# Optimization experiments

Hardware: AMD Instinct MI355X
Metric: run time of the kernel (lower is better)

Reference implementation:

```python
import jax, jax.numpy as jnp
import numpy as np

B, N, D = 4, 2048, 512
H, DA, DL = 8, 64, 64  # heads, attention_dim, linear_dim
EPS = 1e-6


def _layer_norm(x, eps=EPS):
    # F.layer_norm with no affine params
    mu = jnp.mean(x, axis=-1, keepdims=True)
    var = jnp.var(x, axis=-1, keepdims=True)
    return (x - mu) * jax.lax.rsqrt(var + eps)


def setup_inputs() -> dict:
    key = jax.random.key(0)
    k1, k2, k3, k4 = jax.random.split(key, 4)
    x = jax.random.normal(k1, (B, N, D), dtype=jnp.float32)
    # causal (lower-triangular) valid-attention mask, float {0,1}, shape (B,1,N,N)
    attention_mask = jnp.broadcast_to(
        jnp.tril(jnp.ones((N, N), dtype=jnp.float32))[None, None], (B, 1, N, N)
    )
    # _uvqk: (D, 2*H*DL + 2*H*DA), init normal(0, 0.02)
    uvqk = 0.02 * jax.random.normal(k2, (D, 2 * H * DL + 2 * H * DA), dtype=jnp.float32)
    # _o: Linear(H*DL -> D), xavier uniform
    fan_in, fan_out = H * DL, D
    limit = float(np.sqrt(6.0 / (fan_in + fan_out)))
    o_weight = jax.random.uniform(k3, (fan_out, fan_in), dtype=jnp.float32, minval=-limit, maxval=limit)
    o_bias = jnp.zeros((D,), dtype=jnp.float32)
    return {"x": x, "attention_mask": attention_mask, "uvqk": uvqk,
            "o_weight": o_weight, "o_bias": o_bias}


def reference(x, attention_mask, uvqk, o_weight, o_bias):
    b, n, _ = x.shape
    normed_x = _layer_norm(x)
    mm = jax.nn.silu(normed_x @ uvqk)  # fused uvqk projection + silu
    u, v, q, k = jnp.split(mm, [H * DL, 2 * H * DL, 2 * H * DL + H * DA], axis=-1)
    qh = q.reshape(b, n, H, DA)
    kh = k.reshape(b, n, H, DA)
    vh = v.reshape(b, n, H, DL)
    # silu-activated (non-softmax) attention with mask
    qk = jnp.einsum('bnhd,bmhd->bhnm', qh, kh)
    qk = jax.nn.silu(qk) / n
    qk = qk * attention_mask  # (B,1,N,N) broadcast over heads
    attn = jnp.einsum('bhnm,bmhd->bnhd', qk, vh).reshape(b, n, H * DL)
    # gated norm + output proj + residual
    o_input = u * _layer_norm(attn)
    return o_input @ o_weight.T + o_bias + x
```

## Files before the change

### kernel.cpp

```cpp
#include <hip/hip_runtime.h>

typedef __bf16 bf16x8 __attribute__((ext_vector_type(8)));
typedef float f32x4 __attribute__((ext_vector_type(4)));
typedef float f32x16 __attribute__((ext_vector_type(16)));
typedef int i32x2 __attribute__((ext_vector_type(2)));

__device__ __forceinline__ unsigned short f2bf(float f) {
  return __builtin_bit_cast(unsigned short, (__bf16)f);
}
__device__ __forceinline__ float bfu2f(unsigned short b) {
  unsigned int u = ((unsigned int)b) << 16;
  return __builtin_bit_cast(float, u);
}
__device__ __forceinline__ float silu_f(float x) {
  return x * __builtin_amdgcn_rcpf(1.0f + __expf(-x));
}
__device__ __forceinline__ unsigned pk2(float a, float b) {
  return (unsigned)f2bf(a) | ((unsigned)f2bf(b) << 16);
}

template<int CPR, int NI, int SWZ>
__device__ __forceinline__ void stage16(const __bf16* __restrict__ g, int ld,
                                        __bf16* lds, int wave, int lane) {
#pragma unroll
  for (int t = 0; t < NI; ++t) {
    int cb = (wave * NI + t) * 64;
    int c = cb + lane;
    int row = c / CPR;
    int colb = (c % CPR) ^ (row & SWZ);
    __builtin_amdgcn_global_load_lds(
        (const __attribute__((address_space(1))) unsigned int*)(g + row * ld + colb * 8),
        (__attribute__((address_space(3))) unsigned int*)(lds + cb * 8),
        16, 0, 0);
  }
}

__global__ void k_prep(const float* __restrict__ x, __bf16* __restrict__ nx,
                       const float* __restrict__ ow, __bf16* __restrict__ owb,
                       const float* __restrict__ uvqk, __bf16* __restrict__ uvqkT) {
  int bid = blockIdx.x, tid = threadIdx.x;
  if (bid < 4096) {
    int t = tid & 127;
    int r = bid * 2 + (tid >> 7);
    int wave = tid >> 6;
    float4 v = ((const float4*)(x + (size_t)r * 512))[t];
    float s = v.x + v.y + v.z + v.w;
    float ss = v.x * v.x + v.y * v.y + v.z * v.z + v.w * v.w;
#pragma unroll
    for (int o = 32; o > 0; o >>= 1) { s += __shfl_down(s, o); ss += __shfl_down(ss, o); }
    __shared__ float red[4][2];
    if ((tid & 63) == 0) { red[wave][0] = s; red[wave][1] = ss; }
    __syncthreads();
    int rw = (wave >> 1) * 2;
    s = red[rw][0] + red[rw + 1][0];
    ss = red[rw][1] + red[rw + 1][1];
    float mu = s * (1.0f / 512.0f);
    float var = ss * (1.0f / 512.0f) - mu * mu;
    float rs = rsqrtf(var + 1e-6f);
    ushort4 o4;
    o4.x = f2bf((v.x - mu) * rs); o4.y = f2bf((v.y - mu) * rs);
    o4.z = f2bf((v.z - mu) * rs); o4.w = f2bf((v.w - mu) * rs);
    ((ushort4*)(nx + (size_t)r * 512))[t] = o4;
  } else if (bid < 4352) {
    int i = (bid - 4096) * 256 + tid;
    float4 v = ((const float4*)ow)[i];
    ushort4 o4;
    o4.x = f2bf(v.x); o4.y = f2bf(v.y); o4.z = f2bf(v.z); o4.w = f2bf(v.w);
    ((ushort4*)owb)[i] = o4;
  } else {
    __shared__ float tile[32][33];
    int bb = bid - 4352;
    int n0 = (bb & 63) * 32, k0 = (bb >> 6) * 32;
    int tx = tid & 31, ty = tid >> 5;
    for (int i = ty; i < 32; i += 8)
      tile[i][tx] = uvqk[(k0 + i) * 2048 + n0 + tx];
    __syncthreads();
    for (int i = ty; i < 32; i += 8)
      uvqkT[(n0 + i) * 512 + k0 + tx] = (__bf16)tile[tx][i];
  }
}

__global__ __launch_bounds__(256, 2) void k_proj(
    const __bf16* __restrict__ A, const __bf16* __restrict__ Bt,
    __bf16* __restrict__ u, __bf16* __restrict__ qn,
    __bf16* __restrict__ kn, __bf16* __restrict__ vt) {
  __shared__ __bf16 As[128 * 64];
  __shared__ __bf16 Bs[256 * 64];
  int tid = threadIdx.x, wave = tid >> 6, lane = tid & 63;
  int lr = lane & 15, lq = lane >> 4;
  int bn = blockIdx.x, bm = blockIdx.y;
  const __bf16* Ag = A + (size_t)bm * 128 * 512;
  const __bf16* Bg = Bt + (size_t)bn * 256 * 512;
  int wm = (wave >> 1) * 64, wn2 = (wave & 1) * 128;
  f32x4 acc[4][8] = {};
  for (int k0 = 0; k0 < 512; k0 += 64) {
    stage16<8, 4, 7>(Ag + k0, 512, As, wave, lane);
    stage16<8, 8, 7>(Bg + k0, 512, Bs, wave, lane);
    __syncthreads();
#pragma unroll
    for (int kk = 0; kk < 2; ++kk) {
      int b = kk * 4 + lq;
      bf16x8 a[4], bb[8];
#pragma unroll
      for (int i = 0; i < 4; ++i) {
        int row = wm + i * 16 + lr;
        a[i] = *(const bf16x8*)(As + row * 64 + ((b ^ (row & 7)) * 8));
      }
#pragma unroll
      for (int j = 0; j < 8; ++j) {
        int row = wn2 + j * 16 + lr;
        bb[j] = *(const bf16x8*)(Bs + row * 64 + ((b ^ (row & 7)) * 8));
      }
#pragma unroll
      for (int i = 0; i < 4; ++i)
#pragma unroll
        for (int j = 0; j < 8; ++j)
          acc[i][j] = __builtin_amdgcn_mfma_f32_16x16x32_bf16(a[i], bb[j], acc[i][j], 0, 0, 0);
    }
    __syncthreads();
  }
  int seg = bn >> 1;
  int cb = (bn & 1) * 256 + wn2;
  int rb0 = bm * 128 + wm + lq * 4;
  if (seg == 1) {
#pragma unroll
    for (int i = 0; i < 4; ++i) {
      int rb = rb0 + i * 16;
      int b = rb >> 11, n = rb & 2047;
#pragma unroll
      for (int j = 0; j < 8; ++j) {
        int c = cb + j * 16 + lr;
        ushort4 w;
        w.x = f2bf(silu_f(acc[i][j][0]) * (1.0f / 2048.0f));
        w.y = f2bf(silu_f(acc[i][j][1]) * (1.0f / 2048.0f));
        w.z = f2bf(silu_f(acc[i][j][2]) * (1.0f / 2048.0f));
        w.w = f2bf(silu_f(acc[i][j][3]) * (1.0f / 2048.0f));
        *(ushort4*)(vt + ((size_t)(b * 512 + c)) * 2048 + n) = w;
      }
    }
  } else {
    __bf16* dst = (seg == 0) ? u : ((seg == 2) ? qn : kn);
#pragma unroll
    for (int i = 0; i < 4; ++i) {
      int rb = rb0 + i * 16;
#pragma unroll
      for (int j = 0; j < 8; ++j) {
        int c = cb + j * 16 + lr;
#pragma unroll
        for (int rg = 0; rg < 4; ++rg)
          dst[(size_t)(rb + rg) * 512 + c] = (__bf16)silu_f(acc[i][j][rg]);
      }
    }
  }
}

template<bool DT>
__device__ __forceinline__ void attn_finish(
    const f32x16& s, int m0, int n0, int l31, int lh, int ms, bool natural,
    const __bf16* Vc, f32x16 po[2]) {
  unsigned pk[8];
#pragma unroll
  for (int q = 0; q < 8; ++q) {
    float p01[2];
#pragma unroll
    for (int h = 0; h < 2; ++h) {
      int r = 2 * q + h;
      float xx = s[r];
      float pv = xx * __builtin_amdgcn_rcpf(1.0f + __expf(-xx));
      if (DT) {
        int mrow = m0 + 4 * lh + (r & 3) + 8 * (r >> 2);
        if (mrow > n0 + l31) pv = 0.0f;
      }
      p01[h] = pv;
    }
    pk[q] = pk2(p01[0], p01[1]);
  }
  i32x2 r0 = __builtin_amdgcn_permlane32_swap((int)pk[0], (int)pk[2], false, false);
  i32x2 r1 = __builtin_amdgcn_permlane32_swap((int)pk[1], (int)pk[3], false, false);
  i32x2 r2 = __builtin_amdgcn_permlane32_swap((int)pk[4], (int)pk[6], false, false);
  i32x2 r3 = __builtin_amdgcn_permlane32_swap((int)pk[5], (int)pk[7], false, false);
  union { bf16x8 v; unsigned u[4]; } f0, f1;
  if (natural) {
    f0.u[0] = r0.x; f0.u[2] = r0.y; f0.u[1] = r1.x; f0.u[3] = r1.y;
    f1.u[0] = r2.x; f1.u[2] = r2.y; f1.u[1] = r3.x; f1.u[3] = r3.y;
  } else {
    f0.u[0] = r0.y; f0.u[2] = r0.x; f0.u[1] = r1.y; f0.u[3] = r1.x;
    f1.u[0] = r2.y; f1.u[2] = r2.x; f1.u[1] = r3.y; f1.u[3] = r3.x;
  }
  bf16x8 pf[2] = { f0.v, f1.v };
#pragma unroll
  for (int t2 = 0; t2 < 2; ++t2) {
#pragma unroll
    for (int idl = 0; idl < 2; ++idl) {
      int row = idl * 32 + l31;
      bf16x8 av = *(const bf16x8*)(Vc + row * 64 +
          (((ms * 4 + t2 * 2 + lh) ^ (row & 7)) * 8));
      po[idl] = __builtin_amdgcn_mfma_f32_32x32x16_bf16(av, pf[t2], po[idl], 0, 0, 0);
    }
  }
}

__global__ __launch_bounds__(256, 4) void k_attn(
    const __bf16* __restrict__ qn, const __bf16* __restrict__ kn,
    const __bf16* __restrict__ vt, __bf16* __restrict__ oa,
    __bf16* __restrict__ ob, __bf16* __restrict__ oc) {
  __shared__ __bf16 lds[16384];
  __bf16* Kb0 = lds;
  __bf16* Kb1 = lds + 4096;
  __bf16* Vb0 = lds + 8192;
  __bf16* Vb1 = lds + 12288;
  __bf16* bo = lds;

  int bh = blockIdx.x, p = blockIdx.y, z = blockIdx.z;
  int b = bh >> 3, hd = bh & 7;
  int tid = threadIdx.x, wave = tid >> 6, lane = tid & 63;
  int l31 = lane & 31, lh = lane >> 5;
  const __bf16* Kg = kn + (size_t)(b * 2048) * 512 + hd * 64;
  const __bf16* Vg = vt + (size_t)(b * 512 + hd * 64) * 2048;
  __bf16* Oz = (z == 0) ? oa : ((z == 1) ? ob : oc);

  i32x2 pr = __builtin_amdgcn_permlane32_swap(lh ? 10 : 11, lh ? 20 : 21, false, false);
  bool natural = (__builtin_amdgcn_readfirstlane(pr.x) == 11);

  for (int ph = 0; ph < 2; ++ph) {
    int t = ph ? (15 - p) : p;
    int T = 2 * t + 2;
    int mlo = z * T / 3;
    int cnt = (z + 1) * T / 3 - mlo;
    int n0 = t * 128 + wave * 32;
    if (ph) __syncthreads();
    const __bf16* Qg = qn + (size_t)(b * 2048 + n0 + l31) * 512 + hd * 64 + lh * 8;
    bf16x8 qf[4];
#pragma unroll
    for (int ks = 0; ks < 4; ++ks) qf[ks] = *(const bf16x8*)(Qg + ks * 16);
    if (cnt > 0) {
      stage16<8, 2, 7>(Kg + (size_t)mlo * 64 * 512, 512, Kb0, wave, lane);
      stage16<8, 2, 7>(Vg + mlo * 64, 2048, Vb0, wave, lane);
    }
    __syncthreads();

    f32x16 po[2] = {};

    for (int i = 0; i < cnt; ++i) {
      int mt = mlo + i;
      const __bf16* Kc = (i & 1) ? Kb1 : Kb0;
      const __bf16* Vc = (i & 1) ? Vb1 : Vb0;
      if (i + 1 < cnt) {
        __bf16* Kn_ = (i & 1) ? Kb0 : Kb1;
        __bf16* Vn_ = (i & 1) ? Vb0 : Vb1;
        stage16<8, 2, 7>(Kg + (size_t)(mt + 1) * 64 * 512, 512, Kn_, wave, lane);
        stage16<8, 2, 7>(Vg + (mt + 1) * 64, 2048, Vn_, wave, lane);
      }
#pragma unroll
      for (int ms = 0; ms < 2; ++ms) {
        int m0 = mt * 64 + ms * 32;
        if (m0 > n0) continue;
        f32x16 s = {};
#pragma unroll
        for (int ks = 0; ks < 4; ++ks) {
          int row = ms * 32 + l31;
          bf16x8 ak = *(const bf16x8*)(Kc + row * 64 + (((ks * 2 + lh) ^ (row & 7)) * 8));
          s = __builtin_amdgcn_mfma_f32_32x32x16_bf16(ak, qf[ks], s, 0, 0, 0);
        }
        if (m0 == n0) attn_finish<true>(s, m0, n0, l31, lh, ms, natural, Vc, po);
        else          attn_finish<false>(s, m0, n0, l31, lh, ms, natural, Vc, po);
      }
      __syncthreads();
    }

    {
      int nrow = wave * 32 + l31;
#pragma unroll
      for (int idl = 0; idl < 2; ++idl) {
#pragma unroll
        for (int g = 0; g < 4; ++g) {
          int dl0 = idl * 32 + g * 8 + lh * 4;
          int addr = nrow * 64 + ((((dl0 >> 3) ^ (nrow & 7)) << 3) | (dl0 & 7));
          ushort4 w;
          w.x = f2bf(po[idl][4 * g + 0]); w.y = f2bf(po[idl][4 * g + 1]);
          w.z = f2bf(po[idl][4 * g + 2]); w.w = f2bf(po[idl][4 * g + 3]);
          *(ushort4*)(bo + addr) = w;
        }
      }
    }
    __syncthreads();
    {
      int n = tid >> 1, cc = (tid & 1) * 32;
      __bf16* gdst = Oz + (size_t)(b * 2048 + t * 128 + n) * 512 + hd * 64 + cc;
#pragma unroll
      for (int kk2 = 0; kk2 < 4; ++kk2) {
        int dlb = cc + kk2 * 8;
        int a = n * 64 + (((dlb >> 3) ^ (n & 7)) << 3);
        *(uint4*)(gdst + kk2 * 8) = *(const uint4*)(bo + a);
      }
    }
  }
}

__global__ void k_oinput(const __bf16* __restrict__ oa, const __bf16* __restrict__ ob,
                         const __bf16* __restrict__ oc, const __bf16* __restrict__ u,
                         __bf16* __restrict__ oin) {
  int r = blockIdx.x, t = threadIdx.x;
  ushort4 a4 = ((const ushort4*)(oa + (size_t)r * 512))[t];
  ushort4 b4 = ((const ushort4*)(ob + (size_t)r * 512))[t];
  ushort4 c4 = ((const ushort4*)(oc + (size_t)r * 512))[t];
  float a0 = bfu2f(a4.x) + bfu2f(b4.x) + bfu2f(c4.x);
  float a1 = bfu2f(a4.y) + bfu2f(b4.y) + bfu2f(c4.y);
  float a2 = bfu2f(a4.z) + bfu2f(b4.z) + bfu2f(c4.z);
  float a3 = bfu2f(a4.w) + bfu2f(b4.w) + bfu2f(c4.w);
  float s = a0 + a1 + a2 + a3;
  float ss = a0 * a0 + a1 * a1 + a2 * a2 + a3 * a3;
#pragma unroll
  for (int o = 32; o > 0; o >>= 1) { s += __shfl_down(s, o); ss += __shfl_down(ss, o); }
  __shared__ float red[4];
  if ((t & 63) == 0) { red[(t >> 6) * 2] = s; red[(t >> 6) * 2 + 1] = ss; }
  __syncthreads();
  s = red[0] + red[2]; ss = red[1] + red[3];
  float mu = s * (1.0f / 512.0f);
  float var = ss * (1.0f / 512.0f) - mu * mu;
  float rs = rsqrtf(var + 1e-6f);
  ushort4 u4 = ((const ushort4*)(u + (size_t)r * 512))[t];
  ushort4 o4;
  o4.x = f2bf(bfu2f(u4.x) * (a0 - mu) * rs);
  o4.y = f2bf(bfu2f(u4.y) * (a1 - mu) * rs);
  o4.z = f2bf(bfu2f(u4.z) * (a2 - mu) * rs);
  o4.w = f2bf(bfu2f(u4.w) * (a3 - mu) * rs);
  ((ushort4*)(oin + (size_t)r * 512))[t] = o4;
}

__global__ __launch_bounds__(256, 4) void k_out(
    const __bf16* __restrict__ A, const __bf16* __restrict__ Bt,
    const float* __restrict__ bias, const float* __restrict__ x,
    float* __restrict__ out) {
  __shared__ __bf16 As[64 * 64];
  __shared__ __bf16 Bs[128 * 64];
  int tid = threadIdx.x, wave = tid >> 6, lane = tid & 63;
  int lr = lane & 15, lq = lane >> 4;
  int bn = blockIdx.x, bm = blockIdx.y;
  const __bf16* Ag = A + (size_t)bm * 64 * 512;
  const __bf16* Bg = Bt + (size_t)bn * 128 * 512;
  int wm = (wave >> 1) * 32, wn = (wave & 1) * 64;
  f32x4 acc[2][4] = {};
  for (int k0 = 0; k0 < 512; k0 += 64) {
    stage16<8, 2, 7>(Ag + k0, 512, As, wave, lane);
    stage16<8, 4, 7>(Bg + k0, 512, Bs, wave, lane);
    __syncthreads();
#pragma unroll
    for (int kk = 0; kk < 2; ++kk) {
      int b = kk * 4 + lq;
      bf16x8 a[2], bb[4];
#pragma unroll
      for (int i = 0; i < 2; ++i) {
        int row = wm + i * 16 + lr;
        a[i] = *(const bf16x8*)(As + row * 64 + ((b ^ (row & 7)) * 8));
      }
#pragma unroll
      for (int j = 0; j < 4; ++j) {
        int row = wn + j * 16 + lr;
        bb[j] = *(const bf16x8*)(Bs + row * 64 + ((b ^ (row & 7)) * 8));
      }
#pragma unroll
      for (int i = 0; i < 2; ++i)
#pragma unroll
        for (int j = 0; j < 4; ++j)
          acc[i][j] = __builtin_amdgcn_mfma_f32_16x16x32_bf16(a[i], bb[j], acc[i][j], 0, 0, 0);
    }
    __syncthreads();
  }
  int cb = bn * 128 + wn;
  int rb0 = bm * 64 + wm + lq * 4;
#pragma unroll
  for (int j = 0; j < 4; ++j) {
    int c = cb + j * 16 + lr;
    float bv = bias[c];
#pragma unroll
    for (int i = 0; i < 2; ++i) {
      int rb = rb0 + i * 16;
#pragma unroll
      for (int rg = 0; rg < 4; ++rg) {
        size_t idx = (size_t)(rb + rg) * 512 + c;
        out[idx] = acc[i][j][rg] + bv + x[idx];
      }
    }
  }
}

extern "C" void kernel_launch(void* const* d_in, const int* in_sizes, int n_in,
                              void* d_out, int out_size, void* d_ws, size_t ws_size,
                              hipStream_t stream) {
  const float* x = (const float*)d_in[0];
  const float* uvqk = (const float*)d_in[2];
  const float* ow = (const float*)d_in[3];
  const float* obias = (const float*)d_in[4];
  float* out = (float*)d_out;

  char* w = (char*)d_ws;
  const size_t MB8 = 8u * 1024 * 1024;
  __bf16* nx    = (__bf16*)(w);
  __bf16* u     = (__bf16*)(w + MB8);
  __bf16* qn    = (__bf16*)(w + 2 * MB8);
  __bf16* kn    = (__bf16*)(w + 3 * MB8);
  __bf16* vt    = (__bf16*)(w + 4 * MB8);
  __bf16* uvqkT = (__bf16*)(w + 5 * MB8);
  __bf16* owb   = (__bf16*)(w + 5 * MB8 + 2097152);
  __bf16* Oa    = nx;
  __bf16* Ob    = (__bf16*)d_out;
  __bf16* Oc    = (__bf16*)d_out + (size_t)8192 * 512;
  __bf16* o_in  = qn;

  k_prep<<<5376, 256, 0, stream>>>(x, nx, ow, owb, uvqk, uvqkT);
  k_proj<<<dim3(8, 64), 256, 0, stream>>>(nx, uvqkT, u, qn, kn, vt);
  k_attn<<<dim3(32, 8, 3), 256, 0, stream>>>(qn, kn, vt, Oa, Ob, Oc);
  k_oinput<<<8192, 128, 0, stream>>>(Oa, Ob, Oc, u, o_in);
  k_out<<<dim3(4, 128), 256, 0, stream>>>(o_in, owb, obias, x, out);
}
```

Measured before the change: 199.7 us.

## Double-buffer LDS staging in projection and output GEMMs, shrink proj N tile

Both GEMM kernels (k_proj and k_out) now use ping-pong LDS buffers: the next K-slice is issued to global loads while MFMAs run on the current slice, with one barrier per iteration instead of two. k_proj also drops its N tile from 256 to 128 columns, doubling the grid to 1024 blocks to improve CU occupancy and load balance. The aim is to hide global-load latency behind MFMA work. In exchange, each block uses more LDS and k_out's launch bound drops from 4 to 3 blocks per CU, and smaller proj tiles re-read the A operand more often.

```diff
diff --git a/kernel.cpp b/kernel.cpp
--- a/kernel.cpp
+++ b/kernel.cpp
@@ -84,43 +84,57 @@
     const __bf16* __restrict__ A, const __bf16* __restrict__ Bt,
     __bf16* __restrict__ u, __bf16* __restrict__ qn,
     __bf16* __restrict__ kn, __bf16* __restrict__ vt) {
-  __shared__ __bf16 As[128 * 64];
-  __shared__ __bf16 Bs[256 * 64];
+  __shared__ __bf16 lds[32768];
   int tid = threadIdx.x, wave = tid >> 6, lane = tid & 63;
   int lr = lane & 15, lq = lane >> 4;
   int bn = blockIdx.x, bm = blockIdx.y;
   const __bf16* Ag = A + (size_t)bm * 128 * 512;
-  const __bf16* Bg = Bt + (size_t)bn * 256 * 512;
-  int wm = (wave >> 1) * 64, wn2 = (wave & 1) * 128;
-  f32x4 acc[4][8] = {};
-  for (int k0 = 0; k0 < 512; k0 += 64) {
-    stage16<8, 4, 7>(Ag + k0, 512, As, wave, lane);
-    stage16<8, 8, 7>(Bg + k0, 512, Bs, wave, lane);
-    __syncthreads();
+  const __bf16* Bg = Bt + (size_t)bn * 128 * 512;
+  int wm = (wave >> 1) * 64, wn = (wave & 1) * 64;
+  f32x4 acc[4][4] = {};
+  stage16<8, 4, 7>(Ag, 512, lds, wave, lane);
+  stage16<8, 4, 7>(Bg, 512, lds + 8192, wave, lane);
+  asm volatile("s_waitcnt vmcnt(0)" ::: "memory");
+  __builtin_amdgcn_sched_barrier(0);
+  __builtin_amdgcn_s_barrier();
+  __builtin_amdgcn_sched_barrier(0);
+  int buf = 0;
+  for (int t = 0; t < 8; ++t) {
+    if (t + 1 < 8) {
+      int nb = buf ^ 1;
+      stage16<8, 4, 7>(Ag + (t + 1) * 64, 512, lds + nb * 16384, wave, lane);
+      stage16<8, 4, 7>(Bg + (t + 1) * 64, 512, lds + nb * 16384 + 8192, wave, lane);
+    }
+    const __bf16* As = lds + buf * 16384;
+    const __bf16* Bs = lds + buf * 16384 + 8192;
 #pragma unroll
     for (int kk = 0; kk < 2; ++kk) {
       int b = kk * 4 + lq;
-      bf16x8 a[4], bb[8];
+      bf16x8 a[4], bb[4];
 #pragma unroll
       for (int i = 0; i < 4; ++i) {
         int row = wm + i * 16 + lr;
         a[i] = *(const bf16x8*)(As + row * 64 + ((b ^ (row & 7)) * 8));
       }
 #pragma unroll
-      for (int j = 0; j < 8; ++j) {
-        int row = wn2 + j * 16 + lr;
+      for (int j = 0; j < 4; ++j) {
+        int row = wn + j * 16 + lr;
         bb[j] = *(const bf16x8*)(Bs + row * 64 + ((b ^ (row & 7)) * 8));
       }
 #pragma unroll
       for (int i = 0; i < 4; ++i)
 #pragma unroll
-        for (int j = 0; j < 8; ++j)
+        for (int j = 0; j < 4; ++j)
           acc[i][j] = __builtin_amdgcn_mfma_f32_16x16x32_bf16(a[i], bb[j], acc[i][j], 0, 0, 0);
     }
-    __syncthreads();
-  }
-  int seg = bn >> 1;
-  int cb = (bn & 1) * 256 + wn2;
+    asm volatile("s_waitcnt vmcnt(0)" ::: "memory");
+    __builtin_amdgcn_sched_barrier(0);
+    __builtin_amdgcn_s_barrier();
+    __builtin_amdgcn_sched_barrier(0);
+    buf ^= 1;
+  }
+  int seg = bn >> 2;
+  int cb = (bn & 3) * 128 + wn;
   int rb0 = bm * 128 + wm + lq * 4;
   if (seg == 1) {
 #pragma unroll
@@ -128,7 +142,7 @@
       int rb = rb0 + i * 16;
       int b = rb >> 11, n = rb & 2047;
 #pragma unroll
-      for (int j = 0; j < 8; ++j) {
+      for (int j = 0; j < 4; ++j) {
         int c = cb + j * 16 + lr;
         ushort4 w;
         w.x = f2bf(silu_f(acc[i][j][0]) * (1.0f / 2048.0f));
@@ -144,7 +158,7 @@
     for (int i = 0; i < 4; ++i) {
       int rb = rb0 + i * 16;
 #pragma unroll
-      for (int j = 0; j < 8; ++j) {
+      for (int j = 0; j < 4; ++j) {
         int c = cb + j * 16 + lr;
 #pragma unroll
         for (int rg = 0; rg < 4; ++rg)
@@ -328,12 +342,11 @@
   ((ushort4*)(oin + (size_t)r * 512))[t] = o4;
 }
 
-__global__ __launch_bounds__(256, 4) void k_out(
+__global__ __launch_bounds__(256, 3) void k_out(
     const __bf16* __restrict__ A, const __bf16* __restrict__ Bt,
     const float* __restrict__ bias, const float* __restrict__ x,
     float* __restrict__ out) {
-  __shared__ __bf16 As[64 * 64];
-  __shared__ __bf16 Bs[128 * 64];
+  __shared__ __bf16 lds[24576];
   int tid = threadIdx.x, wave = tid >> 6, lane = tid & 63;
   int lr = lane & 15, lq = lane >> 4;
   int bn = blockIdx.x, bm = blockIdx.y;
@@ -341,10 +354,21 @@
   const __bf16* Bg = Bt + (size_t)bn * 128 * 512;
   int wm = (wave >> 1) * 32, wn = (wave & 1) * 64;
   f32x4 acc[2][4] = {};
-  for (int k0 = 0; k0 < 512; k0 += 64) {
-    stage16<8, 2, 7>(Ag + k0, 512, As, wave, lane);
-    stage16<8, 4, 7>(Bg + k0, 512, Bs, wave, lane);
-    __syncthreads();
+  stage16<8, 2, 7>(Ag, 512, lds, wave, lane);
+  stage16<8, 4, 7>(Bg, 512, lds + 4096, wave, lane);
+  asm volatile("s_waitcnt vmcnt(0)" ::: "memory");
+  __builtin_amdgcn_sched_barrier(0);
+  __builtin_amdgcn_s_barrier();
+  __builtin_amdgcn_sched_barrier(0);
+  int buf = 0;
+  for (int t = 0; t < 8; ++t) {
+    if (t + 1 < 8) {
+      int nb = buf ^ 1;
+      stage16<8, 2, 7>(Ag + (t + 1) * 64, 512, lds + nb * 12288, wave, lane);
+      stage16<8, 4, 7>(Bg + (t + 1) * 64, 512, lds + nb * 12288 + 4096, wave, lane);
+    }
+    const __bf16* As = lds + buf * 12288;
+    const __bf16* Bs = lds + buf * 12288 + 4096;
 #pragma unroll
     for (int kk = 0; kk < 2; ++kk) {
       int b = kk * 4 + lq;
@@ -365,7 +389,11 @@
         for (int j = 0; j < 4; ++j)
           acc[i][j] = __builtin_amdgcn_mfma_f32_16x16x32_bf16(a[i], bb[j], acc[i][j], 0, 0, 0);
     }
-    __syncthreads();
+    asm volatile("s_waitcnt vmcnt(0)" ::: "memory");
+    __builtin_amdgcn_sched_barrier(0);
+    __builtin_amdgcn_s_barrier();
+    __builtin_amdgcn_sched_barrier(0);
+    buf ^= 1;
   }
   int cb = bn * 128 + wn;
   int rb0 = bm * 64 + wm + lq * 4;
@@ -409,7 +437,7 @@
   __bf16* o_in  = qn;
 
   k_prep<<<5376, 256, 0, stream>>>(x, nx, ow, owb, uvqk, uvqkT);
-  k_proj<<<dim3(8, 64), 256, 0, stream>>>(nx, uvqkT, u, qn, kn, vt);
+  k_proj<<<dim3(16, 64), 256, 0, stream>>>(nx, uvqkT, u, qn, kn, vt);
   k_attn<<<dim3(32, 8, 3), 256, 0, stream>>>(qn, kn, vt, Oa, Ob, Oc);
   k_oinput<<<8192, 128, 0, stream>>>(Oa, Ob, Oc, u, o_in);
   k_out<<<dim3(4, 128), 256, 0, stream>>>(o_in, owb, obias, x, out);
```

New measurement: 196.9 us, median of 2. No clear change (-1.4%).
